# Optimization experiments

Hardware: AMD Instinct MI355X
Metric: run time of the kernel (lower is better)

The kernel has to match this reference:

```python
import jax, jax.numpy as jnp
import numpy as np

B, S, H, N_IN, N_PROC, R = 4, 1024, 1024, 64, 16, 128

def setup_inputs() -> dict:
    key = jax.random.key(0)
    k0, k1, k2, k3, k4 = jax.random.split(key, 5)
    intermediate = jax.random.normal(k0, (B, S, H), dtype=jnp.float32)
    enriched_activations = jax.random.normal(k1, (B, S, N_IN), dtype=jnp.float32)
    # Conv2d(1 -> N_proc, kernel=(5, N_in)), default PyTorch init scale ~ 1/sqrt(fan_in)
    fan_in = 1 * 5 * N_IN
    conv_w = jax.random.uniform(k2, (N_PROC, 1, 5, N_IN), dtype=jnp.float32,
                                minval=-1.0, maxval=1.0) / np.sqrt(fan_in).astype(np.float32)
    conv_b = jnp.zeros((N_PROC,), dtype=jnp.float32)
    down_proj = 0.02 * jax.random.normal(k3, (N_PROC, H, R), dtype=jnp.float32)
    up_proj = 0.02 * jax.random.normal(k4, (N_PROC, R, H), dtype=jnp.float32)
    return {"intermediate": intermediate, "enriched_activations": enriched_activations,
            "conv_w": conv_w, "conv_b": conv_b, "down_proj": down_proj, "up_proj": up_proj}

def reference(intermediate, enriched_activations, conv_w, conv_b, down_proj, up_proj):
    # act_map: [B, 1, S, N_in]; conv kernel (5, N_in) with padding (2, 0) -> [B, N_proc, S, 1]
    act_map = enriched_activations[:, None, :, :]
    pr = jax.lax.conv_general_dilated(
        act_map, conv_w, window_strides=(1, 1), padding=((2, 2), (0, 0)),
        dimension_numbers=("NCHW", "OIHW", "NCHW"))
    pr = pr + conv_b[None, :, None, None]
    # squeeze width, transpose to [B, S, N_proc], sigmoid gate
    process_activations = jax.nn.sigmoid(jnp.transpose(pr[..., 0], (0, 2, 1)))
    # per-expert low-rank transform
    down = jnp.einsum("bsh,nhr->bsnr", intermediate, down_proj)          # [B,S,N,R]
    transformed = jnp.einsum("bsnr,nrh->bsnh", down, up_proj)            # [B,S,N,H]
    # gate-weighted sum over experts (fuses multiply + sum over n)
    output = jnp.einsum("bsnh,bsn->bsh", transformed, process_activations)
    return (output, process_activations)
```

## Files before the change

kernel.cpp:

```cpp
#include <hip/hip_runtime.h>
#include <hip/hip_fp16.h>

#define T_TOK 4096
#define H_DIM 1024
#define NIN   64
#define NP    16
#define R_DIM 128
#define S_DIM 1024
#define N1    (NP * R_DIM)

typedef _Float16 half8  __attribute__((ext_vector_type(8)));
typedef _Float16 half4v __attribute__((ext_vector_type(4)));
typedef float    floatx4 __attribute__((ext_vector_type(4)));

typedef __attribute__((address_space(3))) unsigned char lds_u8_t;
typedef __attribute__((address_space(1))) unsigned char gbl_u8_t;

__device__ __forceinline__ void g2l16(const void* g, void* l) {
  __builtin_amdgcn_global_load_lds((const gbl_u8_t*)g, (lds_u8_t*)l, 16, 0, 0);
}

#define GATES_NB 256
#define CAST_NB  4096
#define DT_NB    2048
#define UT_NB    2048
#define PREP_NB  (GATES_NB + CAST_NB + DT_NB + UT_NB)

__global__ __launch_bounds__(256)
void prep_kernel(const float* __restrict__ enr, const float* __restrict__ cw,
                 const float* __restrict__ cb, const float* __restrict__ inter,
                 const float* __restrict__ dproj, const float* __restrict__ uproj,
                 float* __restrict__ gates, _Float16* __restrict__ Xh,
                 _Float16* __restrict__ BT1, _Float16* __restrict__ UT) {
  __shared__ __align__(16) char smem_raw[25664];
  const int tid = threadIdx.x;
  int bx = blockIdx.x;

  if (bx < GATES_NB) {
    float (*sw)[321] = (float (*)[321])smem_raw;
    float (*se)[NIN] = (float (*)[NIN])(smem_raw + 20544);
    const int t0 = bx * 16;
    const int b = t0 / S_DIM, s0 = t0 % S_DIM;
    for (int i = tid; i < NP * 320; i += 256) sw[i / 320][i % 320] = cw[i];
    for (int i = tid; i < 20 * NIN; i += 256) {
      int r = i >> 6, c = i & 63, s = s0 + r - 2;
      se[r][c] = (s >= 0 && s < S_DIM) ? enr[((size_t)b * S_DIM + s) * NIN + c] : 0.f;
    }
    __syncthreads();
    const int lt = tid >> 4, n = tid & 15;
    float acc = cb[n];
    #pragma unroll
    for (int dh = 0; dh < 5; ++dh) {
      const float* wrow = &sw[n][dh * 64];
      const float* erow = se[lt + dh];
      #pragma unroll
      for (int j = 0; j < NIN; ++j) acc += erow[j] * wrow[j];
    }
    gates[(size_t)(t0 + lt) * NP + n] = 1.f / (1.f + expf(-acc));
    return;
  }
  bx -= GATES_NB;
  if (bx < CAST_NB) {
    int i = bx * 256 + tid;
    float4 v = reinterpret_cast<const float4*>(inter)[i];
    half4v o;
    o[0] = (_Float16)v.x; o[1] = (_Float16)v.y; o[2] = (_Float16)v.z; o[3] = (_Float16)v.w;
    reinterpret_cast<half4v*>(Xh)[i] = o;
    return;
  }
  bx -= CAST_NB;
  const float* src; _Float16* dst; int rows, cols, bxt, byt;
  if (bx < DT_NB) {
    int n = bx >> 7, rem = bx & 127;
    src = dproj + (size_t)n * H_DIM * R_DIM;
    dst = BT1 + (size_t)n * R_DIM * H_DIM;
    rows = H_DIM; cols = R_DIM; bxt = rem & 3; byt = rem >> 2;
  } else {
    bx -= DT_NB;
    src = uproj; dst = UT; rows = N1; cols = H_DIM;
    bxt = bx & 31; byt = bx >> 5;
  }
  float (*tile)[33] = (float (*)[33])smem_raw;
  const int c0 = bxt * 32, r0 = byt * 32;
  const int tx = tid & 31, ty = tid >> 5;
  #pragma unroll
  for (int k = 0; k < 32; k += 8)
    tile[ty + k][tx] = src[(size_t)(r0 + ty + k) * cols + c0 + tx];
  __syncthreads();
  #pragma unroll
  for (int k = 0; k < 32; k += 8)
    dst[(size_t)(c0 + ty + k) * rows + r0 + tx] = (_Float16)tile[tx][ty + k];
}

template <int BM, int GATE>
__global__ __launch_bounds__(256)
void gemm_bt(const _Float16* __restrict__ A, const _Float16* __restrict__ BT,
             const float* __restrict__ gates, void* __restrict__ Cv,
             const int N, const int K) {
  constexpr int BN = 128, BK = 64;
  constexpr int WM = BM / 2, WN = BN / 2;
  constexpr int MI = WM / 16, NJ = WN / 16;
  constexpr int CA = BM / 32, CB = BN / 32;
  __shared__ _Float16 sA[BM * BK];
  __shared__ _Float16 sB[BN * BK];

  const int tid = threadIdx.x, wave = tid >> 6, lane = tid & 63;
  const int m0 = blockIdx.y * BM, n0 = blockIdx.x * BN;
  const int wr = (wave >> 1) * WM, wc = (wave & 1) * WN;
  const int rl = lane >> 3;
  const int q  = (lane & 7) ^ rl;
  const int fr = lane & 15, quad = lane >> 4;

  const _Float16* gA = A  + (size_t)(m0 + wave * CA * 8 + rl) * K + q * 8;
  const _Float16* gB = BT + (size_t)(n0 + wave * CB * 8 + rl) * K + q * 8;
  _Float16* lA = sA + wave * CA * 512;
  _Float16* lB = sB + wave * CB * 512;

  floatx4 acc[MI][NJ];
  #pragma unroll
  for (int i = 0; i < MI; ++i)
    #pragma unroll
    for (int j = 0; j < NJ; ++j) acc[i][j] = (floatx4)0.f;

  for (int k0 = 0; k0 < K; k0 += BK) {
    __syncthreads();
    #pragma unroll
    for (int c = 0; c < CA; ++c) g2l16(gA + (size_t)c * 8 * K + k0, lA + c * 512);
    #pragma unroll
    for (int c = 0; c < CB; ++c) g2l16(gB + (size_t)c * 8 * K + k0, lB + c * 512);
    __syncthreads();
    #pragma unroll
    for (int h = 0; h < 2; ++h) {
      const int sa = ((quad + 4 * h) ^ (fr & 7)) * 8;
      half8 af[MI], bf[NJ];
      #pragma unroll
      for (int i = 0; i < MI; ++i)
        af[i] = *reinterpret_cast<const half8*>(&sA[(wr + i * 16 + fr) * 64 + sa]);
      #pragma unroll
      for (int j = 0; j < NJ; ++j)
        bf[j] = *reinterpret_cast<const half8*>(&sB[(wc + j * 16 + fr) * 64 + sa]);
      #pragma unroll
      for (int i = 0; i < MI; ++i)
        #pragma unroll
        for (int j = 0; j < NJ; ++j)
          acc[i][j] = __builtin_amdgcn_mfma_f32_16x16x32_f16(af[i], bf[j], acc[i][j], 0, 0, 0);
    }
  }

  if (GATE) {
    _Float16* C = (_Float16*)Cv;
    #pragma unroll
    for (int i = 0; i < MI; ++i)
      #pragma unroll
      for (int r = 0; r < 4; ++r) {
        const int row = m0 + wr + i * 16 + quad * 4 + r;
        const float g = gates[row * NP + blockIdx.x];
        #pragma unroll
        for (int j = 0; j < NJ; ++j)
          C[(size_t)row * N + n0 + wc + j * 16 + fr] = (_Float16)(acc[i][j][r] * g);
      }
  } else {
    float* C = (float*)Cv;
    #pragma unroll
    for (int i = 0; i < MI; ++i)
      #pragma unroll
      for (int r = 0; r < 4; ++r) {
        const int row = m0 + wr + i * 16 + quad * 4 + r;
        #pragma unroll
        for (int j = 0; j < NJ; ++j)
          C[(size_t)row * N + n0 + wc + j * 16 + fr] = acc[i][j][r];
      }
  }
}

extern "C" void kernel_launch(void* const* d_in, const int* in_sizes, int n_in,
                              void* d_out, int out_size, void* d_ws, size_t ws_size,
                              hipStream_t stream) {
  const float* inter = (const float*)d_in[0];
  const float* enr   = (const float*)d_in[1];
  const float* convw = (const float*)d_in[2];
  const float* convb = (const float*)d_in[3];
  const float* dproj = (const float*)d_in[4];
  const float* uproj = (const float*)d_in[5];
  float* out   = (float*)d_out;
  float* gates = out + (size_t)T_TOK * H_DIM;

  _Float16* Xh  = (_Float16*)d_ws;
  _Float16* BT1 = Xh  + (size_t)T_TOK * H_DIM;
  _Float16* UT  = BT1 + (size_t)N1 * H_DIM;
  _Float16* Dsc = UT  + (size_t)H_DIM * N1;

  prep_kernel<<<PREP_NB, 256, 0, stream>>>(enr, convw, convb, inter, dproj, uproj,
                                           gates, Xh, BT1, UT);
  gemm_bt<128, 1><<<dim3(N1 / 128, T_TOK / 128), 256, 0, stream>>>(
      Xh, BT1, gates, (void*)Dsc, N1, H_DIM);
  gemm_bt<64, 0><<<dim3(H_DIM / 128, T_TOK / 64), 256, 0, stream>>>(
      Dsc, UT, nullptr, (void*)out, H_DIM, N1);
}
```

Baseline: 146.4 us.

## Switch GEMMs to 32x32x16 MFMA with BK=128 and staged gate values

Both GEMM kernels move from 16x16x32 MFMA tiles to 32x32x16 MFMA tiles, which changes the accumulator layout, the fragment indexing and the epilogue row mapping. The K-tile doubles to 128 with a matching XOR swizzle for the LDS loads, halving the number of barrier/load iterations. Gate values are preloaded into shared memory instead of being read from global memory per row in the epilogue. The larger LDS footprint per block may reduce occupancy, and the loop is still single-buffered.

New measurement: 139.8 us. -4.5%, faster.

```diff
diff --git a/kernel.cpp b/kernel.cpp
--- a/kernel.cpp
+++ b/kernel.cpp
@@ -11,7 +11,7 @@
 
 typedef _Float16 half8  __attribute__((ext_vector_type(8)));
 typedef _Float16 half4v __attribute__((ext_vector_type(4)));
-typedef float    floatx4 __attribute__((ext_vector_type(4)));
+typedef float    floatx16 __attribute__((ext_vector_type(16)));
 
 typedef __attribute__((address_space(3))) unsigned char lds_u8_t;
 typedef __attribute__((address_space(1))) unsigned char gbl_u8_t;
@@ -92,58 +92,65 @@
     dst[(size_t)(c0 + ty + k) * rows + r0 + tx] = (_Float16)tile[tx][ty + k];
 }
 
-template <int BM, int GATE>
+template <int BM, int BN, int GATE>
 __global__ __launch_bounds__(256)
 void gemm_bt(const _Float16* __restrict__ A, const _Float16* __restrict__ BT,
              const float* __restrict__ gates, void* __restrict__ Cv,
              const int N, const int K) {
-  constexpr int BN = 128, BK = 64;
+  constexpr int BK = 128, NCH = BK / 8;
+  constexpr int RPC = 64 / NCH;
   constexpr int WM = BM / 2, WN = BN / 2;
-  constexpr int MI = WM / 16, NJ = WN / 16;
-  constexpr int CA = BM / 32, CB = BN / 32;
+  constexpr int MI = WM / 32, NJ = WN / 32;
+  constexpr int CA = BM * BK / 2048, CB = BN * BK / 2048;
   __shared__ _Float16 sA[BM * BK];
   __shared__ _Float16 sB[BN * BK];
+  __shared__ float sg[BM];
 
   const int tid = threadIdx.x, wave = tid >> 6, lane = tid & 63;
   const int m0 = blockIdx.y * BM, n0 = blockIdx.x * BN;
   const int wr = (wave >> 1) * WM, wc = (wave & 1) * WN;
-  const int rl = lane >> 3;
-  const int q  = (lane & 7) ^ rl;
-  const int fr = lane & 15, quad = lane >> 4;
-
-  const _Float16* gA = A  + (size_t)(m0 + wave * CA * 8 + rl) * K + q * 8;
-  const _Float16* gB = BT + (size_t)(n0 + wave * CB * 8 + rl) * K + q * 8;
-  _Float16* lA = sA + wave * CA * 512;
-  _Float16* lB = sB + wave * CB * 512;
-
-  floatx4 acc[MI][NJ];
+  const int rl = lane >> 4;
+  const int ql = lane & 15;
+  const int r = lane & 31, kh = lane >> 5;
+
+  if (GATE && tid < BM) sg[tid] = gates[(size_t)(m0 + tid) * NP + blockIdx.x];
+
+  floatx16 acc[MI][NJ];
   #pragma unroll
   for (int i = 0; i < MI; ++i)
     #pragma unroll
-    for (int j = 0; j < NJ; ++j) acc[i][j] = (floatx4)0.f;
+    for (int j = 0; j < NJ; ++j) acc[i][j] = (floatx16)0.f;
 
   for (int k0 = 0; k0 < K; k0 += BK) {
     __syncthreads();
     #pragma unroll
-    for (int c = 0; c < CA; ++c) g2l16(gA + (size_t)c * 8 * K + k0, lA + c * 512);
-    #pragma unroll
-    for (int c = 0; c < CB; ++c) g2l16(gB + (size_t)c * 8 * K + k0, lB + c * 512);
+    for (int c = 0; c < CA; ++c) {
+      const int rowL = wave * CA * RPC + c * RPC + rl;
+      const int q = ql ^ (rowL & (NCH - 1));
+      g2l16(A + (size_t)(m0 + rowL) * K + k0 + q * 8, sA + (size_t)rowL * BK);
+    }
+    #pragma unroll
+    for (int c = 0; c < CB; ++c) {
+      const int rowL = wave * CB * RPC + c * RPC + rl;
+      const int q = ql ^ (rowL & (NCH - 1));
+      g2l16(BT + (size_t)(n0 + rowL) * K + k0 + q * 8, sB + (size_t)rowL * BK);
+    }
     __syncthreads();
     #pragma unroll
-    for (int h = 0; h < 2; ++h) {
-      const int sa = ((quad + 4 * h) ^ (fr & 7)) * 8;
+    for (int h = 0; h < BK / 16; ++h) {
+      const int p8 = (((2 * h + kh) ^ (r & 15))) * 8;
       half8 af[MI], bf[NJ];
       #pragma unroll
       for (int i = 0; i < MI; ++i)
-        af[i] = *reinterpret_cast<const half8*>(&sA[(wr + i * 16 + fr) * 64 + sa]);
+        af[i] = *reinterpret_cast<const half8*>(&sA[(wr + i * 32 + r) * BK + p8]);
       #pragma unroll
       for (int j = 0; j < NJ; ++j)
-        bf[j] = *reinterpret_cast<const half8*>(&sB[(wc + j * 16 + fr) * 64 + sa]);
+        bf[j] = *reinterpret_cast<const half8*>(&sB[(wc + j * 32 + r) * BK + p8]);
       #pragma unroll
       for (int i = 0; i < MI; ++i)
         #pragma unroll
         for (int j = 0; j < NJ; ++j)
-          acc[i][j] = __builtin_amdgcn_mfma_f32_16x16x32_f16(af[i], bf[j], acc[i][j], 0, 0, 0);
+          acc[i][j] = __builtin_amdgcn_mfma_f32_32x32x16_f16(af[i], bf[j], acc[i][j], 0, 0, 0);
     }
   }
 
@@ -152,24 +159,29 @@
     #pragma unroll
     for (int i = 0; i < MI; ++i)
       #pragma unroll
-      for (int r = 0; r < 4; ++r) {
-        const int row = m0 + wr + i * 16 + quad * 4 + r;
-        const float g = gates[row * NP + blockIdx.x];
+      for (int g4 = 0; g4 < 4; ++g4)
         #pragma unroll
-        for (int j = 0; j < NJ; ++j)
-          C[(size_t)row * N + n0 + wc + j * 16 + fr] = (_Float16)(acc[i][j][r] * g);
-      }
+        for (int rr = 0; rr < 4; ++rr) {
+          const int rowL = wr + i * 32 + rr + 8 * g4 + 4 * kh;
+          const float g = sg[rowL];
+          #pragma unroll
+          for (int j = 0; j < NJ; ++j)
+            C[(size_t)(m0 + rowL) * N + n0 + wc + j * 32 + r] =
+                (_Float16)(acc[i][j][g4 * 4 + rr] * g);
+        }
   } else {
     float* C = (float*)Cv;
     #pragma unroll
     for (int i = 0; i < MI; ++i)
       #pragma unroll
-      for (int r = 0; r < 4; ++r) {
-        const int row = m0 + wr + i * 16 + quad * 4 + r;
+      for (int g4 = 0; g4 < 4; ++g4)
         #pragma unroll
-        for (int j = 0; j < NJ; ++j)
-          C[(size_t)row * N + n0 + wc + j * 16 + fr] = acc[i][j][r];
-      }
+        for (int rr = 0; rr < 4; ++rr) {
+          const int rowL = wr + i * 32 + rr + 8 * g4 + 4 * kh;
+          #pragma unroll
+          for (int j = 0; j < NJ; ++j)
+            C[(size_t)(m0 + rowL) * N + n0 + wc + j * 32 + r] = acc[i][j][g4 * 4 + rr];
+        }
   }
 }
 
@@ -192,8 +204,8 @@
 
   prep_kernel<<<PREP_NB, 256, 0, stream>>>(enr, convw, convb, inter, dproj, uproj,
                                            gates, Xh, BT1, UT);
-  gemm_bt<128, 1><<<dim3(N1 / 128, T_TOK / 128), 256, 0, stream>>>(
+  gemm_bt<128, 128, 1><<<dim3(N1 / 128, T_TOK / 128), 256, 0, stream>>>(
       Xh, BT1, gates, (void*)Dsc, N1, H_DIM);
-  gemm_bt<64, 0><<<dim3(H_DIM / 128, T_TOK / 64), 256, 0, stream>>>(
+  gemm_bt<64, 128, 0><<<dim3(H_DIM / 128, T_TOK / 64), 256, 0, stream>>>(
       Dsc, UT, nullptr, (void*)out, H_DIM, N1);
 }
```
